# Performance work log

Measured on AMD Instinct MI355X. Metric: run time of the kernel, lower is better.

## Reference

```python
import jax, jax.numpy as jnp
import numpy as np
import math

DX = DZ = DATTN = DOUT = 1024
LX = LZ = 4096

def setup_inputs() -> dict:
    key = jax.random.key(0)
    ks = jax.random.split(key, 6)
    X = jax.random.normal(ks[0], (DX, LX), dtype=jnp.float32)
    Z = jax.random.normal(ks[1], (DZ, LZ), dtype=jnp.float32)
    mask = jax.random.randint(ks[2], (LZ, LX), 0, 2) > 0  # bool (lz, lx)
    Wq = jax.random.normal(ks[3], (DATTN, DX), dtype=jnp.float32) / math.sqrt(DATTN)
    bq = jnp.zeros((DATTN, 1), dtype=jnp.float32)
    Wk = jax.random.normal(ks[4], (DATTN, DZ), dtype=jnp.float32) / math.sqrt(DATTN)
    bk = jnp.zeros((DATTN, 1), dtype=jnp.float32)
    Wv = jax.random.normal(ks[5], (DOUT, DZ), dtype=jnp.float32) / math.sqrt(DOUT)
    bv = jnp.zeros((DOUT, 1), dtype=jnp.float32)
    return {"X": X, "Z": Z, "mask": mask, "Wq": Wq, "bq": bq,
            "Wk": Wk, "bk": bk, "Wv": Wv, "bv": bv}

def reference(X, Z, mask, Wq, bq, Wk, bk, Wv, bv):
    dattn_sqrt = math.sqrt(Wq.shape[0])
    q = Wq @ X + bq                      # (dattn, lx)
    k = Wk @ Z + bk                      # (dattn, lz)
    v = Wv @ Z + bv                      # (dout, lz)
    score = k.T @ q                      # (lz, lx)
    # masked_fill with -1000 happens BEFORE scaling, matching the original
    score = jnp.where(mask, score, jnp.float32(-1000.0))
    attn = jax.nn.softmax(score / dattn_sqrt, axis=0)  # softmax over lz (dim 0)
    return v @ attn                      # (dout, lx)
```

## Files before the change

kernel.cpp:

```cpp
#include <hip/hip_runtime.h>
#include <hip/hip_bf16.h>
#include <math.h>

constexpr int DXc = 1024;
constexpr int DZc = 1024;
constexpr int LXc = 4096;
constexpr int LZc = 4096;
constexpr int DAc = 1024;
constexpr int DOc = 1024;

typedef __attribute__((ext_vector_type(8))) short bf16x8;
typedef __attribute__((ext_vector_type(4))) float f32x4;

__device__ __forceinline__ ushort f2bf(float f) {
    __hip_bfloat16 h = __float2bfloat16(f);
    return *reinterpret_cast<ushort*>(&h);
}

enum BiasMode { BIAS_NONE, BIAS_M, BIAS_N };

#define SCHED0() __builtin_amdgcn_sched_barrier(0)
#define BAR2()   do { SCHED0(); __builtin_amdgcn_s_barrier(); SCHED0(); } while (0)
#define LGKM0()  do { asm volatile("s_waitcnt lgkmcnt(0)" ::: "memory"); SCHED0(); } while (0)
#define VMCNT(n) do { asm volatile("s_waitcnt vmcnt(" #n ")" ::: "memory"); SCHED0(); } while (0)

template<BiasMode BMODE, bool OUT_BF16, bool ATOMICOUT, bool EXPEPI>
__device__ __forceinline__ void gemm256(
    const ushort* __restrict__ A, const ushort* __restrict__ B,
    const float* __restrict__ bias, void* __restrict__ Cv,
    int M, int N, int K, int lda, int ldb, int ldc,
    int m0, int n0, int kbase, char* smem,
    const unsigned* __restrict__ bits, float* __restrict__ sums)
{
    const int tid  = threadIdx.x;
    const int wid  = tid >> 6, lane = tid & 63;
    const int wr   = wid >> 2, wc = wid & 3;
    const int lrow = lane & 15, quad = lane >> 4;
    const int swz  = (lrow & 7) << 4;
    const int cx0  = (quad * 16) ^ swz;
    const int cx1  = (64 + quad * 16) ^ swz;
    const int raB  = (wr * 16 + lrow) * 128;
    const int rbB  = (wc * 16 + lrow) * 128;

    char* const Ab0 = smem;
    char* const Ab1 = smem + 32768;
    char* const Bb0 = smem + 65536;
    char* const Bb1 = smem + 98304;

    auto stage = [&](const ushort* __restrict__ Mat, int ld, int r0, int kc,
                     char* dstBuf, int h) {
        #pragma unroll
        for (int r = 0; r < 2; ++r) {
            const int q = h * 16384 + r * 8192 + wid * 1024 + lane * 16;
            const int p = q ^ (((q >> 7) & 7) << 4);
            const ushort* g = Mat + (size_t)(r0 + (p >> 7)) * ld + kc + ((p & 127) >> 1);
            __builtin_amdgcn_global_load_lds(
                (const __attribute__((address_space(1))) void*)g,
                (__attribute__((address_space(3))) void*)(dstBuf + h * 16384 + r * 8192 + wid * 1024),
                16, 0, 0);
        }
    };

    f32x4  acc[8][4] = {};
    bf16x8 alo[4][2], ahi[4][2], blo[2][2], bhi[2][2];

    auto ldLo = [&](char* Abuf, char* Bbuf) {
        #pragma unroll
        for (int m = 0; m < 4; ++m) {
            alo[m][0] = *reinterpret_cast<const bf16x8*>(Abuf + m * 4096 + raB + cx0);
            alo[m][1] = *reinterpret_cast<const bf16x8*>(Abuf + m * 4096 + raB + cx1);
        }
        #pragma unroll
        for (int n = 0; n < 2; ++n) {
            blo[n][0] = *reinterpret_cast<const bf16x8*>(Bbuf + n * 8192 + rbB + cx0);
            blo[n][1] = *reinterpret_cast<const bf16x8*>(Bbuf + n * 8192 + rbB + cx1);
        }
    };
    auto ldAhi = [&](char* Abuf) {
        #pragma unroll
        for (int m = 0; m < 4; ++m) {
            ahi[m][0] = *reinterpret_cast<const bf16x8*>(Abuf + (m + 4) * 4096 + raB + cx0);
            ahi[m][1] = *reinterpret_cast<const bf16x8*>(Abuf + (m + 4) * 4096 + raB + cx1);
        }
    };
    auto ldBhi = [&](char* Bbuf) {
        #pragma unroll
        for (int n = 0; n < 2; ++n) {
            bhi[n][0] = *reinterpret_cast<const bf16x8*>(Bbuf + (n + 2) * 8192 + rbB + cx0);
            bhi[n][1] = *reinterpret_cast<const bf16x8*>(Bbuf + (n + 2) * 8192 + rbB + cx1);
        }
    };
    auto mmaQ = [&](bf16x8 (&a)[4][2], bf16x8 (&b)[2][2], int mh, int nh) {
        __builtin_amdgcn_s_setprio(1);
        #pragma unroll
        for (int m = 0; m < 4; ++m)
            #pragma unroll
            for (int n = 0; n < 2; ++n) {
                f32x4& c = acc[mh * 4 + m][nh * 2 + n];
                c = __builtin_amdgcn_mfma_f32_16x16x32_bf16(a[m][0], b[n][0], c, 0, 0, 0);
                c = __builtin_amdgcn_mfma_f32_16x16x32_bf16(a[m][1], b[n][1], c, 0, 0, 0);
            }
        __builtin_amdgcn_s_setprio(0);
    };

    const int NIT = K >> 7;

    stage(A, lda, m0, kbase,      Ab0, 0);
    stage(B, ldb, n0, kbase,      Bb0, 0);
    stage(B, ldb, n0, kbase,      Bb0, 1);
    stage(A, lda, m0, kbase,      Ab0, 1);
    VMCNT(4);
    stage(A, lda, m0, kbase + 64, Ab1, 0);
    stage(B, ldb, n0, kbase + 64, Bb1, 0);
    stage(B, ldb, n0, kbase + 64, Bb1, 1);
    VMCNT(6);
    BAR2();

    #pragma unroll 1
    for (int it = 0; it < NIT; ++it) {
        const bool st  = (it < NIT - 1);
        const int kU   = kbase + (2 * it + 1) * 64;
        const int kT2  = kbase + (2 * it + 2) * 64;
        const int kT3  = kbase + (2 * it + 3) * 64;

        ldLo(Ab0, Bb0);
        stage(A, lda, m0, kU, Ab1, 1);
        asm volatile("s_waitcnt lgkmcnt(8)" ::: "memory");
        BAR2(); LGKM0();
        mmaQ(alo, blo, 0, 0);
        BAR2();
        ldBhi(Bb0);
        if (st) stage(A, lda, m0, kT2, Ab0, 0);
        BAR2(); LGKM0();
        mmaQ(alo, bhi, 0, 1);
        BAR2();
        ldAhi(Ab0);
        if (st) stage(B, ldb, n0, kT2, Bb0, 0);
        BAR2(); LGKM0();
        mmaQ(ahi, bhi, 1, 1);
        BAR2();
        if (st) { stage(B, ldb, n0, kT2, Bb0, 1); VMCNT(6); }
        else    { VMCNT(0); }
        BAR2();
        mmaQ(ahi, blo, 1, 0);
        BAR2();
        ldLo(Ab1, Bb1);
        if (st) stage(A, lda, m0, kT2, Ab0, 1);
        asm volatile("s_waitcnt lgkmcnt(8)" ::: "memory");
        BAR2(); LGKM0();
        mmaQ(alo, blo, 0, 0);
        BAR2();
        ldBhi(Bb1);
        if (st) stage(A, lda, m0, kT3, Ab1, 0);
        BAR2(); LGKM0();
        mmaQ(alo, bhi, 0, 1);
        BAR2();
        ldAhi(Ab1);
        if (st) stage(B, ldb, n0, kT3, Bb1, 0);
        BAR2(); LGKM0();
        mmaQ(ahi, bhi, 1, 1);
        BAR2();
        if (st) { stage(B, ldb, n0, kT3, Bb1, 1); VMCNT(6); }
        else    { VMCNT(0); }
        BAR2();
        mmaQ(ahi, blo, 1, 0);
        BAR2();
    }

    if (EXPEPI) {
        constexpr float scale = 1.0f / 32.0f;
        constexpr float MASKV = -1000.0f / 32.0f;
        ushort* Cb = (ushort*)Cv;
        #pragma unroll
        for (int m = 0; m < 8; ++m) {
            const int rowb = m0 + 32 * m + wr * 16 + quad * 4;
            #pragma unroll
            for (int r = 0; r < 4; ++r) {
                const int row = rowb + r;
                const unsigned* bw = bits + (size_t)row * (LZc / 32);
                float rp = 0.0f;
                #pragma unroll
                for (int n = 0; n < 4; ++n) {
                    const int col = n0 + 64 * n + wc * 16 + lrow;
                    const unsigned wbm = bw[col >> 5];
                    const float sv = ((wbm >> (col & 31)) & 1u)
                                         ? acc[m][n][r] * scale : MASKV;
                    const float e = __expf(sv);
                    rp += e;
                    Cb[(size_t)row * ldc + col] = f2bf(e);
                }
                rp += __shfl_xor(rp, 1, 64);
                rp += __shfl_xor(rp, 2, 64);
                rp += __shfl_xor(rp, 4, 64);
                rp += __shfl_xor(rp, 8, 64);
                if (lrow == 0) atomicAdd(&sums[row], rp);
            }
        }
        return;
    }
    if (ATOMICOUT) {
        float* Co = (float*)Cv;
        float dinv[4];
        #pragma unroll
        for (int n = 0; n < 4; ++n)
            dinv[n] = 1.0f / sums[n0 + 64 * n + wc * 16 + lrow];
        #pragma unroll
        for (int m = 0; m < 8; ++m) {
            const int rowb = m0 + 32 * m + wr * 16 + quad * 4;
            #pragma unroll
            for (int r = 0; r < 4; ++r) {
                const int row = rowb + r;
                #pragma unroll
                for (int n = 0; n < 4; ++n) {
                    const int col = n0 + 64 * n + wc * 16 + lrow;
                    atomicAdd(&Co[(size_t)row * ldc + col], acc[m][n][r] * dinv[n]);
                }
            }
        }
        return;
    }
    ushort* Cb = (ushort*)Cv;
    #pragma unroll
    for (int m = 0; m < 8; ++m) {
        const int rowb = m0 + 32 * m + wr * 16 + quad * 4;
        #pragma unroll
        for (int r = 0; r < 4; ++r) {
            const int row = rowb + r;
            const float bm = (BMODE == BIAS_M) ? bias[row] : 0.0f;
            #pragma unroll
            for (int n = 0; n < 4; ++n) {
                const int col = n0 + 64 * n + wc * 16 + lrow;
                float v = acc[m][n][r] + ((BMODE == BIAS_N) ? bias[col] : bm);
                Cb[(size_t)row * ldc + col] = f2bf(v);
            }
        }
    }
}

__global__ __launch_bounds__(512, 2)
void proj256_kernel(const ushort* __restrict__ XT, const ushort* __restrict__ ZT,
                    const ushort* __restrict__ Wqb, const ushort* __restrict__ Wkb,
                    const ushort* __restrict__ Wvb,
                    const float* __restrict__ bq, const float* __restrict__ bk,
                    const float* __restrict__ bv,
                    ushort* __restrict__ qT, ushort* __restrict__ kT,
                    ushort* __restrict__ vB)
{
    extern __shared__ char smem[];
    int b = blockIdx.x;
    if (b < 64) {
        gemm256<BIAS_N, true, false, false>(XT, Wqb, bq, qT, LXc, DAc, DXc, DXc, DXc, DAc,
                                            (b >> 2) * 256, (b & 3) * 256, 0, smem,
                                            nullptr, nullptr);
    } else if (b < 128) {
        b -= 64;
        gemm256<BIAS_N, true, false, false>(ZT, Wkb, bk, kT, LZc, DAc, DZc, DZc, DZc, DAc,
                                            (b >> 2) * 256, (b & 3) * 256, 0, smem,
                                            nullptr, nullptr);
    } else {
        b -= 128;
        gemm256<BIAS_M, true, false, false>(Wvb, ZT, bv, vB, DOc, LZc, DZc, DZc, DZc, LZc,
                                            (b >> 4) * 256, (b & 15) * 256, 0, smem,
                                            nullptr, nullptr);
    }
}

__global__ __launch_bounds__(512, 2)
void score256_kernel(const ushort* __restrict__ qT, const ushort* __restrict__ kT,
                     ushort* __restrict__ sTb, const unsigned* __restrict__ bits,
                     float* __restrict__ sums)
{
    extern __shared__ char smem[];
    const int b = blockIdx.x;
    gemm256<BIAS_NONE, true, false, true>(qT, kT, nullptr, sTb, LXc, LZc, DAc, DAc, DAc, LZc,
                                          (b >> 4) * 256, (b & 15) * 256, 0, smem,
                                          bits, sums);
}

__global__ __launch_bounds__(512, 2)
void out256_kernel(const ushort* __restrict__ vB, const ushort* __restrict__ sTb,
                   float* __restrict__ sums, float* __restrict__ out)
{
    extern __shared__ char smem[];
    gemm256<BIAS_NONE, false, true, false>(vB, sTb, nullptr, out, DOc, LXc, LZc / 4,
                                           LZc, LZc, LXc,
                                           blockIdx.y * 256, blockIdx.x * 256,
                                           blockIdx.z * (LZc / 4), smem,
                                           nullptr, sums);
}

__global__ __launch_bounds__(256)
void prep_kernel(const float* __restrict__ X, const float* __restrict__ Z,
                 const float* __restrict__ Wq, const float* __restrict__ Wk,
                 const float* __restrict__ Wv, const int* __restrict__ mask,
                 ushort* __restrict__ XT, ushort* __restrict__ ZT,
                 ushort* __restrict__ Wqb, ushort* __restrict__ Wkb,
                 ushort* __restrict__ Wvb, unsigned* __restrict__ bits,
                 float* __restrict__ sums, float* __restrict__ outz)
{
    __shared__ float tile[32][33];
    const int tid = threadIdx.x;
    int b = blockIdx.x;

    if (b < 8192) {
        const float* in  = (b < 4096) ? X : Z;
        ushort*      out = (b < 4096) ? XT : ZT;
        const int local = b & 4095;
        const int bx = local & 127, by = local >> 7;
        const int c0 = bx * 32, r0 = by * 32;
        const int tx = tid & 31, ty = tid >> 5;
        #pragma unroll
        for (int i = 0; i < 32; i += 8)
            tile[ty + i][tx] = in[(size_t)(r0 + ty + i) * LXc + c0 + tx];
        __syncthreads();
        #pragma unroll
        for (int i = 0; i < 32; i += 8)
            out[(size_t)(c0 + ty + i) * DXc + r0 + tx] = f2bf(tile[tx][ty + i]);
        return;
    }
    if (b < 11264) {
        b -= 8192;
        const float* in  = (b < 1024) ? Wq : (b < 2048) ? Wk : Wv;
        ushort*      out = (b < 1024) ? Wqb : (b < 2048) ? Wkb : Wvb;
        const int local = b & 1023;
        const size_t i = ((size_t)local * 256 + tid) * 4;
        float4 f = *reinterpret_cast<const float4*>(in + i);
        ushort4 u;
        u.x = f2bf(f.x); u.y = f2bf(f.y); u.z = f2bf(f.z); u.w = f2bf(f.w);
        *reinterpret_cast<ushort4*>(out + i) = u;
        return;
    }
    if (b < 13312) {
        b -= 11264;
        const int xb = b & 15, zb = b >> 4;
        const int x  = xb * 256 + tid;
        const int z0 = zb * 32;
        unsigned w = 0;
        #pragma unroll 8
        for (int i = 0; i < 32; ++i)
            w |= (mask[(size_t)(z0 + i) * LXc + x] != 0 ? 1u : 0u) << i;
        bits[(size_t)x * (LZc / 32) + zb] = w;
        return;
    }
    if (b < 17408) {
        b -= 13312;
        const size_t i = ((size_t)b * 256 + tid) * 4;
        float4 z4 = {0.0f, 0.0f, 0.0f, 0.0f};
        *reinterpret_cast<float4*>(outz + i) = z4;
        return;
    }
    float4 z4 = {0.0f, 0.0f, 0.0f, 0.0f};
    #pragma unroll
    for (int i = 0; i < 4; ++i)
        *reinterpret_cast<float4*>(sums + (size_t)tid * 16 + i * 4) = z4;
}

extern "C" void kernel_launch(void* const* d_in, const int* in_sizes, int n_in,
                              void* d_out, int out_size, void* d_ws, size_t ws_size,
                              hipStream_t stream)
{
    const float* X    = (const float*)d_in[0];
    const float* Z    = (const float*)d_in[1];
    const int*   mask = (const int*)  d_in[2];
    const float* Wq   = (const float*)d_in[3];
    const float* bq   = (const float*)d_in[4];
    const float* Wk   = (const float*)d_in[5];
    const float* bk   = (const float*)d_in[6];
    const float* Wv   = (const float*)d_in[7];
    const float* bv   = (const float*)d_in[8];
    float* out = (float*)d_out;

    static bool inited = false;
    if (!inited) {
        (void)hipFuncSetAttribute((const void*)proj256_kernel,
                                  hipFuncAttributeMaxDynamicSharedMemorySize, 131072);
        (void)hipFuncSetAttribute((const void*)score256_kernel,
                                  hipFuncAttributeMaxDynamicSharedMemorySize, 131072);
        (void)hipFuncSetAttribute((const void*)out256_kernel,
                                  hipFuncAttributeMaxDynamicSharedMemorySize, 131072);
        inited = true;
    }

    char* ws = (char*)d_ws;
    ushort*   XT   = (ushort*)(ws);
    ushort*   ZT   = (ushort*)(ws + ( 8ull << 20));
    ushort*   Wqb  = (ushort*)(ws + (16ull << 20));
    ushort*   Wkb  = (ushort*)(ws + (18ull << 20));
    ushort*   Wvb  = (ushort*)(ws + (20ull << 20));
    ushort*   qT   = (ushort*)(ws + (22ull << 20));
    ushort*   kT   = (ushort*)(ws + (30ull << 20));
    unsigned* bits = (unsigned*)(ws + (38ull << 20));
    ushort*   vB   = (ushort*)(ws + (64ull << 20));
    ushort*   sTb  = (ushort*)(ws + (72ull << 20));
    float*    sums = (float*) (ws + (104ull << 20));

    prep_kernel<<<dim3(17409), 256, 0, stream>>>(X, Z, Wq, Wk, Wv, mask,
                                                 XT, ZT, Wqb, Wkb, Wvb, bits,
                                                 sums, out);
    proj256_kernel<<<dim3(192), 512, 131072, stream>>>(XT, ZT, Wqb, Wkb, Wvb,
                                                       bq, bk, bv, qT, kT, vB);
    score256_kernel<<<dim3(256), 512, 131072, stream>>>(qT, kT, sTb, bits, sums);
    out256_kernel<<<dim3(16, 4, 4), 512, 131072, stream>>>(vB, sTb, sums, out);
}
```

Before: 321.7 us.

## Replace atomic split-K output and softmax sums with partial buffers plus reduction

```diff
diff --git a/kernel.cpp b/kernel.cpp
--- a/kernel.cpp
+++ b/kernel.cpp
@@ -11,6 +11,7 @@
 
 typedef __attribute__((ext_vector_type(8))) short bf16x8;
 typedef __attribute__((ext_vector_type(4))) float f32x4;
+typedef __attribute__((ext_vector_type(8))) _Float16 f16x8;
 
 __device__ __forceinline__ ushort f2bf(float f) {
     __hip_bfloat16 h = __float2bfloat16(f);
@@ -18,19 +19,20 @@
 }
 
 enum BiasMode { BIAS_NONE, BIAS_M, BIAS_N };
+enum EpiMode  { EPI_BF16, EPI_EXP, EPI_F16DIV };
 
 #define SCHED0() __builtin_amdgcn_sched_barrier(0)
 #define BAR2()   do { SCHED0(); __builtin_amdgcn_s_barrier(); SCHED0(); } while (0)
 #define LGKM0()  do { asm volatile("s_waitcnt lgkmcnt(0)" ::: "memory"); SCHED0(); } while (0)
 #define VMCNT(n) do { asm volatile("s_waitcnt vmcnt(" #n ")" ::: "memory"); SCHED0(); } while (0)
 
-template<BiasMode BMODE, bool OUT_BF16, bool ATOMICOUT, bool EXPEPI>
+template<BiasMode BMODE, EpiMode EPI>
 __device__ __forceinline__ void gemm256(
     const ushort* __restrict__ A, const ushort* __restrict__ B,
     const float* __restrict__ bias, void* __restrict__ Cv,
     int M, int N, int K, int lda, int ldb, int ldc,
-    int m0, int n0, int kbase, char* smem,
-    const unsigned* __restrict__ bits, float* __restrict__ sums)
+    int m0, int n0, int kbase, int zsplit, char* smem,
+    const unsigned* __restrict__ bits, float* __restrict__ S)
 {
     const int tid  = threadIdx.x;
     const int wid  = tid >> 6, lane = tid & 63;
@@ -167,10 +169,11 @@
         BAR2();
     }
 
-    if (EXPEPI) {
+    if (EPI == EPI_EXP) {
         constexpr float scale = 1.0f / 32.0f;
         constexpr float MASKV = -1000.0f / 32.0f;
         ushort* Cb = (ushort*)Cv;
+        float* Srow = S + (size_t)((n0 >> 8) * 4 + wc) * LXc;
         #pragma unroll
         for (int m = 0; m < 8; ++m) {
             const int rowb = m0 + 32 * m + wr * 16 + quad * 4;
@@ -193,17 +196,22 @@
                 rp += __shfl_xor(rp, 2, 64);
                 rp += __shfl_xor(rp, 4, 64);
                 rp += __shfl_xor(rp, 8, 64);
-                if (lrow == 0) atomicAdd(&sums[row], rp);
+                if (lrow == 0) Srow[row] = rp;
             }
         }
         return;
     }
-    if (ATOMICOUT) {
-        float* Co = (float*)Cv;
+    if (EPI == EPI_F16DIV) {
+        _Float16* Ch = (_Float16*)Cv + (size_t)zsplit * (size_t)M * ldc;
         float dinv[4];
         #pragma unroll
-        for (int n = 0; n < 4; ++n)
-            dinv[n] = 1.0f / sums[n0 + 64 * n + wc * 16 + lrow];
+        for (int n = 0; n < 4; ++n) {
+            const int col = n0 + 64 * n + wc * 16 + lrow;
+            float s = 0.0f;
+            #pragma unroll 16
+            for (int j = 0; j < 64; ++j) s += S[(size_t)j * LXc + col];
+            dinv[n] = 1.0f / s;
+        }
         #pragma unroll
         for (int m = 0; m < 8; ++m) {
             const int rowb = m0 + 32 * m + wr * 16 + quad * 4;
@@ -213,7 +221,7 @@
                 #pragma unroll
                 for (int n = 0; n < 4; ++n) {
                     const int col = n0 + 64 * n + wc * 16 + lrow;
-                    atomicAdd(&Co[(size_t)row * ldc + col], acc[m][n][r] * dinv[n]);
+                    Ch[(size_t)row * ldc + col] = (_Float16)(acc[m][n][r] * dinv[n]);
                 }
             }
         }
@@ -249,44 +257,44 @@
     extern __shared__ char smem[];
     int b = blockIdx.x;
     if (b < 64) {
-        gemm256<BIAS_N, true, false, false>(XT, Wqb, bq, qT, LXc, DAc, DXc, DXc, DXc, DAc,
-                                            (b >> 2) * 256, (b & 3) * 256, 0, smem,
-                                            nullptr, nullptr);
+        gemm256<BIAS_N, EPI_BF16>(XT, Wqb, bq, qT, LXc, DAc, DXc, DXc, DXc, DAc,
+                                  (b >> 2) * 256, (b & 3) * 256, 0, 0, smem,
+                                  nullptr, nullptr);
     } else if (b < 128) {
         b -= 64;
-        gemm256<BIAS_N, true, false, false>(ZT, Wkb, bk, kT, LZc, DAc, DZc, DZc, DZc, DAc,
-                                            (b >> 2) * 256, (b & 3) * 256, 0, smem,
-                                            nullptr, nullptr);
+        gemm256<BIAS_N, EPI_BF16>(ZT, Wkb, bk, kT, LZc, DAc, DZc, DZc, DZc, DAc,
+                                  (b >> 2) * 256, (b & 3) * 256, 0, 0, smem,
+                                  nullptr, nullptr);
     } else {
         b -= 128;
-        gemm256<BIAS_M, true, false, false>(Wvb, ZT, bv, vB, DOc, LZc, DZc, DZc, DZc, LZc,
-                                            (b >> 4) * 256, (b & 15) * 256, 0, smem,
-                                            nullptr, nullptr);
+        gemm256<BIAS_M, EPI_BF16>(Wvb, ZT, bv, vB, DOc, LZc, DZc, DZc, DZc, LZc,
+                                  (b >> 4) * 256, (b & 15) * 256, 0, 0, smem,
+                                  nullptr, nullptr);
     }
 }
 
 __global__ __launch_bounds__(512, 2)
 void score256_kernel(const ushort* __restrict__ qT, const ushort* __restrict__ kT,
                      ushort* __restrict__ sTb, const unsigned* __restrict__ bits,
-                     float* __restrict__ sums)
+                     float* __restrict__ S)
 {
     extern __shared__ char smem[];
     const int b = blockIdx.x;
-    gemm256<BIAS_NONE, true, false, true>(qT, kT, nullptr, sTb, LXc, LZc, DAc, DAc, DAc, LZc,
-                                          (b >> 4) * 256, (b & 15) * 256, 0, smem,
-                                          bits, sums);
+    gemm256<BIAS_NONE, EPI_EXP>(qT, kT, nullptr, sTb, LXc, LZc, DAc, DAc, DAc, LZc,
+                                (b >> 4) * 256, (b & 15) * 256, 0, 0, smem,
+                                bits, S);
 }
 
 __global__ __launch_bounds__(512, 2)
 void out256_kernel(const ushort* __restrict__ vB, const ushort* __restrict__ sTb,
-                   float* __restrict__ sums, float* __restrict__ out)
+                   _Float16* __restrict__ P, float* __restrict__ S)
 {
     extern __shared__ char smem[];
-    gemm256<BIAS_NONE, false, true, false>(vB, sTb, nullptr, out, DOc, LXc, LZc / 4,
-                                           LZc, LZc, LXc,
-                                           blockIdx.y * 256, blockIdx.x * 256,
-                                           blockIdx.z * (LZc / 4), smem,
-                                           nullptr, sums);
+    gemm256<BIAS_NONE, EPI_F16DIV>(vB, sTb, nullptr, P, DOc, LXc, LZc / 4,
+                                   LZc, LZc, LXc,
+                                   blockIdx.y * 256, blockIdx.x * 256,
+                                   blockIdx.z * (LZc / 4), blockIdx.z, smem,
+                                   nullptr, S);
 }
 
 __global__ __launch_bounds__(256)
@@ -295,8 +303,7 @@
                  const float* __restrict__ Wv, const int* __restrict__ mask,
                  ushort* __restrict__ XT, ushort* __restrict__ ZT,
                  ushort* __restrict__ Wqb, ushort* __restrict__ Wkb,
-                 ushort* __restrict__ Wvb, unsigned* __restrict__ bits,
-                 float* __restrict__ sums, float* __restrict__ outz)
+                 ushort* __restrict__ Wvb, unsigned* __restrict__ bits)
 {
     __shared__ float tile[32][33];
     const int tid = threadIdx.x;
@@ -330,29 +337,33 @@
         *reinterpret_cast<ushort4*>(out + i) = u;
         return;
     }
-    if (b < 13312) {
-        b -= 11264;
-        const int xb = b & 15, zb = b >> 4;
-        const int x  = xb * 256 + tid;
-        const int z0 = zb * 32;
-        unsigned w = 0;
-        #pragma unroll 8
-        for (int i = 0; i < 32; ++i)
-            w |= (mask[(size_t)(z0 + i) * LXc + x] != 0 ? 1u : 0u) << i;
-        bits[(size_t)x * (LZc / 32) + zb] = w;
-        return;
-    }
-    if (b < 17408) {
-        b -= 13312;
-        const size_t i = ((size_t)b * 256 + tid) * 4;
-        float4 z4 = {0.0f, 0.0f, 0.0f, 0.0f};
-        *reinterpret_cast<float4*>(outz + i) = z4;
-        return;
-    }
-    float4 z4 = {0.0f, 0.0f, 0.0f, 0.0f};
+    b -= 11264;
+    const int xb = b & 15, zb = b >> 4;
+    const int x  = xb * 256 + tid;
+    const int z0 = zb * 32;
+    unsigned w = 0;
+    #pragma unroll 8
+    for (int i = 0; i < 32; ++i)
+        w |= (mask[(size_t)(z0 + i) * LXc + x] != 0 ? 1u : 0u) << i;
+    bits[(size_t)x * (LZc / 32) + zb] = w;
+}
+
+__global__ __launch_bounds__(256)
+void reduce_kernel(const _Float16* __restrict__ P, float* __restrict__ out)
+{
+    constexpr size_t total = (size_t)DOc * LXc;
+    const size_t i = ((size_t)blockIdx.x * 256 + threadIdx.x) * 8;
+    float s[8] = {};
     #pragma unroll
-    for (int i = 0; i < 4; ++i)
-        *reinterpret_cast<float4*>(sums + (size_t)tid * 16 + i * 4) = z4;
+    for (int p = 0; p < 4; ++p) {
+        const f16x8 t = *reinterpret_cast<const f16x8*>(P + (size_t)p * total + i);
+        #pragma unroll
+        for (int j = 0; j < 8; ++j) s[j] += (float)t[j];
+    }
+    float4 o0 = {s[0], s[1], s[2], s[3]};
+    float4 o1 = {s[4], s[5], s[6], s[7]};
+    *reinterpret_cast<float4*>(out + i)     = o0;
+    *reinterpret_cast<float4*>(out + i + 4) = o1;
 }
 
 extern "C" void kernel_launch(void* const* d_in, const int* in_sizes, int n_in,
@@ -389,16 +400,17 @@
     ushort*   Wvb  = (ushort*)(ws + (20ull << 20));
     ushort*   qT   = (ushort*)(ws + (22ull << 20));
     ushort*   kT   = (ushort*)(ws + (30ull << 20));
-    unsigned* bits = (unsigned*)(ws + (38ull << 20));
+    _Float16* P    = (_Float16*)(ws);
+    float*    S    = (float*) (ws + (40ull << 20));
     ushort*   vB   = (ushort*)(ws + (64ull << 20));
     ushort*   sTb  = (ushort*)(ws + (72ull << 20));
-    float*    sums = (float*) (ws + (104ull << 20));
-
-    prep_kernel<<<dim3(17409), 256, 0, stream>>>(X, Z, Wq, Wk, Wv, mask,
-                                                 XT, ZT, Wqb, Wkb, Wvb, bits,
-                                                 sums, out);
+    unsigned* bits = (unsigned*)(ws + (104ull << 20));
+
+    prep_kernel<<<dim3(13312), 256, 0, stream>>>(X, Z, Wq, Wk, Wv, mask,
+                                                 XT, ZT, Wqb, Wkb, Wvb, bits);
     proj256_kernel<<<dim3(192), 512, 131072, stream>>>(XT, ZT, Wqb, Wkb, Wvb,
                                                        bq, bk, bv, qT, kT, vB);
-    score256_kernel<<<dim3(256), 512, 131072, stream>>>(qT, kT, sTb, bits, sums);
-    out256_kernel<<<dim3(16, 4, 4), 512, 131072, stream>>>(vB, sTb, sums, out);
-}
+    score256_kernel<<<dim3(256), 512, 131072, stream>>>(qT, kT, sTb, bits, S);
+    out256_kernel<<<dim3(16, 4, 4), 512, 131072, stream>>>(vB, sTb, P, S);
+    reduce_kernel<<<dim3(DOc * LXc / 2048), 256, 0, stream>>>(P, out);
+}
```

After: 284.4 us. 1.13x faster.
